# Optimization experiments

Hardware: AMD Instinct MI355X
Metric: run time of the kernel (lower is better)

Reference implementation:

```python
import jax, jax.numpy as jnp
import numpy as np

B, S, D = 2, 2048, 1024
H, DQK, DV = 16, 64, 64
DECAY = 0.85


def _fractal_weights(seq_len: int, decay: float) -> np.ndarray:
    # Dragon-curve hierarchical weights: earlier (coarser) positions get higher
    # weight; weight decays by `decay` per hierarchy level. Normalized to sum 1,
    # matching DragonCurveGenerator.get_hierarchical_weights semantics.
    idx = np.arange(seq_len)
    level = np.floor(np.log2(idx + 1)).astype(np.int32)
    w = decay ** level.astype(np.float32)
    return (w / w.sum()).astype(np.float32)


def setup_inputs() -> dict:
    key = jax.random.key(0)
    kx, kq, kk, kv, ko = jax.random.split(key, 5)
    s = 1.0 / np.sqrt(D)
    return {
        "x": jax.random.normal(kx, (B, S, D), dtype=jnp.float32),
        "Wq": jax.random.normal(kq, (D, H * DQK), dtype=jnp.float32) * s,
        "Wk": jax.random.normal(kk, (D, H * DQK), dtype=jnp.float32) * s,
        "Wv": jax.random.normal(kv, (D, H * DV), dtype=jnp.float32) * s,
        "Wo": jax.random.normal(ko, (H * DV, D), dtype=jnp.float32) * s,
        "fractal_weights": jnp.asarray(_fractal_weights(S, DECAY)),
    }


def reference(x, Wq, Wk, Wv, Wo, fractal_weights):
    b, s, _ = x.shape
    # Projections (Linear with bias=False); weights stored as (in, out).
    Q = (x @ Wq).reshape(b, s, H, DQK).transpose(0, 2, 1, 3)  # [B,H,S,Dqk]
    K = (x @ Wk).reshape(b, s, H, DQK).transpose(0, 2, 1, 3)
    V = (x @ Wv).reshape(b, s, H, DV).transpose(0, 2, 1, 3)   # [B,H,S,Dv]
    scale = 1.0 / jnp.sqrt(jnp.asarray(DQK, dtype=x.dtype))
    scores = jnp.einsum("bhqd,bhkd->bhqk", Q, K) * scale      # [B,H,S,S]
    # Multiplicative per-key fractal bias applied BEFORE softmax.
    scores = scores * fractal_weights[None, None, None, :]
    attn = jax.nn.softmax(scores, axis=-1)
    out = jnp.einsum("bhqk,bhkd->bhqd", attn, V)               # [B,H,S,Dv]
    out = out.transpose(0, 2, 1, 3).reshape(b, s, H * DV)
    return out @ Wo                                            # [B,S,D]
```

## Files before the change

### kernel.cpp

```cpp
#include <hip/hip_runtime.h>
#include <hip/hip_bf16.h>
#include <stdint.h>

#define B_  2
#define S_  2048
#define D_  1024
#define H_  16
#define DH_ 64

typedef __attribute__((ext_vector_type(8))) __bf16    bf16x8;
typedef __attribute__((ext_vector_type(8))) _Float16  f16x8;
typedef __attribute__((ext_vector_type(4))) _Float16  f16x4;
typedef __attribute__((ext_vector_type(2))) __fp16    fp16x2;
typedef __attribute__((ext_vector_type(4))) float     f32x4;

__device__ inline unsigned short f2bf(float f) {
    union { float f; uint32_t u; } v; v.f = f;
    uint32_t r = (v.u + 0x7fffu + ((v.u >> 16) & 1u)) >> 16;
    return (unsigned short)r;
}

__device__ __forceinline__ void g2l16(const unsigned short* g, unsigned short* l) {
    __builtin_amdgcn_global_load_lds(
        (const __attribute__((address_space(1))) unsigned int*)g,
        (__attribute__((address_space(3))) unsigned int*)l,
        16, 0, 0);
}


__global__ void convert_x(const float* __restrict__ x, unsigned short* __restrict__ xb, int n) {
    int i = (blockIdx.x * blockDim.x + threadIdx.x) * 4;
    if (i < n) {
        float4 v = *(const float4*)(x + i);
        ushort4 o;
        o.x = f2bf(v.x); o.y = f2bf(v.y); o.z = f2bf(v.z); o.w = f2bf(v.w);
        *(ushort4*)(xb + i) = o;
    }
}

__global__ void transpose_w(const float* __restrict__ s0, const float* __restrict__ s1,
                            const float* __restrict__ s2, const float* __restrict__ s3,
                            unsigned short* __restrict__ d0, unsigned short* __restrict__ d1,
                            unsigned short* __restrict__ d2, unsigned short* __restrict__ d3) {
    __shared__ float tile[32][33];
    const float* src; unsigned short* dst;
    switch (blockIdx.z) {
        case 0: src = s0; dst = d0; break;
        case 1: src = s1; dst = d1; break;
        case 2: src = s2; dst = d2; break;
        default: src = s3; dst = d3; break;
    }
    int n0 = blockIdx.x * 32, k0 = blockIdx.y * 32;
    int tx = threadIdx.x, ty = threadIdx.y;
    for (int j = 0; j < 32; j += 8)
        tile[ty + j][tx] = src[(long)(k0 + ty + j) * 1024 + n0 + tx];
    __syncthreads();
    for (int j = 0; j < 32; j += 8)
        dst[(long)(n0 + ty + j) * 1024 + k0 + tx] = f2bf(tile[tx][ty + j]);
}

__global__ __launch_bounds__(256, 2)
void gemm128(const unsigned short* __restrict__ A, const unsigned short* __restrict__ Bt,
             unsigned short* __restrict__ Qo, unsigned short* __restrict__ Ko,
             unsigned short* __restrict__ Vt,
             const float* __restrict__ fw)
{
    __shared__ __align__(16) unsigned short As[128 * 64];
    __shared__ __align__(16) unsigned short Bs[128 * 64];
    const int tid  = threadIdx.x;
    const int lane = tid & 63, wid = tid >> 6;
    const int quad = lane >> 4, l15 = lane & 15;
    const int wm = wid >> 1, wn = wid & 1;
    const int bm = blockIdx.y, bn = blockIdx.x;
    const int K = 1024;
    f32x4 acc[4][4] = {};
    const long Abase = (long)bm * 128 * K;
    const long Bbase = (long)bn * 128 * K;

    for (int k0 = 0; k0 < K; k0 += 64) {
        __syncthreads();
#pragma unroll
        for (int i = 0; i < 4; i++) {
            int slot = i * 256 + wid * 64 + lane;
            int row = slot >> 3, cp = slot & 7;
            int c = cp ^ (row & 7);
            g2l16(A + Abase + (long)row * K + k0 + c * 8, &As[(i * 256 + wid * 64) * 8]);
        }
#pragma unroll
        for (int i = 0; i < 4; i++) {
            int slot = i * 256 + wid * 64 + lane;
            int row = slot >> 3, cp = slot & 7;
            int c = cp ^ (row & 7);
            g2l16(Bt + Bbase + (long)row * K + k0 + c * 8, &Bs[(i * 256 + wid * 64) * 8]);
        }
        __syncthreads();
#pragma unroll
        for (int ks = 0; ks < 2; ks++) {
            bf16x8 af[4], bfr[4];
#pragma unroll
            for (int t = 0; t < 4; t++) {
                int ra = wm * 64 + t * 16 + l15;
                af[t]  = *(const bf16x8*)(As + ra * 64 + (((ks * 4 + quad) ^ (l15 & 7))) * 8);
                int rb = wn * 64 + t * 16 + l15;
                bfr[t] = *(const bf16x8*)(Bs + rb * 64 + (((ks * 4 + quad) ^ (l15 & 7))) * 8);
            }
#pragma unroll
            for (int tm = 0; tm < 4; tm++)
#pragma unroll
                for (int tn = 0; tn < 4; tn++)
                    acc[tm][tn] = __builtin_amdgcn_mfma_f32_16x16x32_bf16(af[tm], bfr[tn], acc[tm][tn], 0, 0, 0);
        }
    }

    const float Cq = 0.125f * 1.44269504f;
    for (int tm = 0; tm < 4; tm++)
        for (int tn = 0; tn < 4; tn++)
            for (int r = 0; r < 4; r++) {
                int gm = bm * 128 + wm * 64 + tm * 16 + quad * 4 + r;
                int gn = bn * 128 + wn * 64 + tn * 16 + l15;
                float v = acc[tm][tn][r];
                int b = gm >> 11, s = gm & 2047;
                if (gn < 1024) {
                    int h = gn >> 6, d = gn & 63;
                    Qo[(((long)(b * H_ + h) * S_ + s) << 6) + d] = f2bf(v * Cq);
                } else if (gn < 2048) {
                    int g = gn - 1024; int h = g >> 6, d = g & 63;
                    Ko[(((long)(b * H_ + h) * S_ + s) << 6) + d] = f2bf(v * fw[s]);
                } else {
                    int g = gn - 2048; int h = g >> 6, d = g & 63;
                    union { _Float16 h; unsigned short u; } cv;
                    cv.h = (_Float16)v;
                    int sp = s ^ ((d & 8) ? 4 : 0);
                    Vt[((long)(b * H_ + h) * DH_ + d) * S_ + sp] = cv.u;
                }
            }
}

__global__ __launch_bounds__(256, 2)
void gemm_wo(const unsigned short* __restrict__ A, const unsigned short* __restrict__ Bt,
             float* __restrict__ Cout)
{
    __shared__ __align__(16) unsigned short As[128 * 64];
    __shared__ __align__(16) unsigned short Bs[64 * 64];
    const int tid  = threadIdx.x;
    const int lane = tid & 63, wid = tid >> 6;
    const int quad = lane >> 4, l15 = lane & 15;
    const int bm = blockIdx.y, bn = blockIdx.x;
    const int K = 1024;
    f32x4 acc[2][4] = {};
    const long Abase = (long)bm * 128 * K;
    const long Bbase = (long)bn * 64 * K;

    for (int k0 = 0; k0 < K; k0 += 64) {
        __syncthreads();
#pragma unroll
        for (int i = 0; i < 4; i++) {
            int slot = i * 256 + wid * 64 + lane;
            int row = slot >> 3, cp = slot & 7;
            int c = cp ^ (row & 7);
            g2l16(A + Abase + (long)row * K + k0 + c * 8, &As[(i * 256 + wid * 64) * 8]);
        }
#pragma unroll
        for (int i = 0; i < 2; i++) {
            int slot = i * 256 + wid * 64 + lane;
            int row = slot >> 3, cp = slot & 7;
            int c = cp ^ (row & 7);
            g2l16(Bt + Bbase + (long)row * K + k0 + c * 8, &Bs[(i * 256 + wid * 64) * 8]);
        }
        __syncthreads();
#pragma unroll
        for (int ks = 0; ks < 2; ks++) {
            bf16x8 af[2], bfr[4];
#pragma unroll
            for (int t = 0; t < 2; t++) {
                int ra = wid * 32 + t * 16 + l15;
                af[t]  = *(const bf16x8*)(As + ra * 64 + (((ks * 4 + quad) ^ (l15 & 7))) * 8);
            }
#pragma unroll
            for (int t = 0; t < 4; t++) {
                int rb = t * 16 + l15;
                bfr[t] = *(const bf16x8*)(Bs + rb * 64 + (((ks * 4 + quad) ^ (l15 & 7))) * 8);
            }
#pragma unroll
            for (int tm = 0; tm < 2; tm++)
#pragma unroll
                for (int tn = 0; tn < 4; tn++)
                    acc[tm][tn] = __builtin_amdgcn_mfma_f32_16x16x32_bf16(af[tm], bfr[tn], acc[tm][tn], 0, 0, 0);
        }
    }

    for (int tm = 0; tm < 2; tm++)
        for (int tn = 0; tn < 4; tn++)
            for (int r = 0; r < 4; r++) {
                int gm = bm * 128 + wid * 32 + tm * 16 + quad * 4 + r;
                int gn = bn * 64 + tn * 16 + l15;
                Cout[(long)gm * 1024 + gn] = acc[tm][tn][r];
            }
}

__global__ __launch_bounds__(512, 4)
void attn_kernel(const unsigned short* __restrict__ Q, const unsigned short* __restrict__ Kb,
                 const unsigned short* __restrict__ Vt,
                 unsigned short* __restrict__ O)
{
    __shared__ __align__(16) unsigned short smem[2][2][2][64 * 64];

    const int tid  = threadIdx.x;
    const int lane = tid & 63, wid = tid >> 6;
    const int half = wid >> 2, sw = wid & 3;
    const int quad = lane >> 4, l15 = lane & 15;
    const int bh = blockIdx.y;
    const int qt = blockIdx.x;

    const unsigned short* Kg = Kb + (long)bh * S_ * DH_;
    const unsigned short* Vg = Vt + (long)bh * (long)DH_ * S_;

    bf16x8 qf[2][2];
#pragma unroll
    for (int st = 0; st < 2; st++) {
        const unsigned short* Qp = Q + ((long)bh * S_ + qt * 128 + sw * 32 + st * 16 + l15) * DH_ + quad * 8;
        qf[st][0] = *(const bf16x8*)(Qp);
        qf[st][1] = *(const bf16x8*)(Qp + 32);
    }

    auto issue = [&](int buf, int kt) {
#pragma unroll
        for (int i = 0; i < 2; i++) {
            int base = i * 256 + sw * 64;
            int slot = base + lane;
            int row = slot >> 3, cp = slot & 7;
            int c = cp ^ (row & 7);
            g2l16(Kg + ((long)(kt * 64 + row) * 64 + c * 8), &smem[half][buf][0][base * 8]);
        }
#pragma unroll
        for (int i = 0; i < 2; i++) {
            int base = i * 256 + sw * 64;
            int slot = base + lane;
            int row = slot >> 3, cp = slot & 7;
            int c = cp ^ (row & 7);
            g2l16(Vg + ((long)row * S_ + kt * 64 + c * 8), &smem[half][buf][1][base * 8]);
        }
    };

    f32x4 oacc[2][4] = {};
    f32x4 lacc[2] = {};
    const f16x8 vone = {(_Float16)1.f, (_Float16)1.f, (_Float16)1.f, (_Float16)1.f,
                        (_Float16)1.f, (_Float16)1.f, (_Float16)1.f, (_Float16)1.f};

    const int kt0 = half * 16;
    issue(0, kt0);
    __syncthreads();

    const int hf = (((quad & 1) ^ ((l15 >> 3) & 1))) * 4;

    for (int t = 0; t < 16; t++) {
        const int cur = t & 1;
        if (t + 1 < 16) issue(1 - cur, kt0 + t + 1);

        const unsigned short* Kc = &smem[half][cur][0][0];
        const unsigned short* Vc = &smem[half][cur][1][0];

        f32x4 sacc[2][4] = {};
#pragma unroll
        for (int kc = 0; kc < 4; kc++) {
            int row = kc * 16 + l15;
            bf16x8 k0 = *(const bf16x8*)(Kc + (row * 8 + (quad       ^ (l15 & 7))) * 8);
            bf16x8 k1 = *(const bf16x8*)(Kc + (row * 8 + ((4 + quad) ^ (l15 & 7))) * 8);
#pragma unroll
            for (int st = 0; st < 2; st++) {
                sacc[st][kc] = __builtin_amdgcn_mfma_f32_16x16x32_bf16(k0, qf[st][0], sacc[st][kc], 0, 0, 0);
                sacc[st][kc] = __builtin_amdgcn_mfma_f32_16x16x32_bf16(k1, qf[st][1], sacc[st][kc], 0, 0, 0);
            }
        }

        f16x8 vfr[2][4];
#pragma unroll
        for (int c = 0; c < 2; c++)
#pragma unroll
            for (int dt = 0; dt < 4; dt++) {
                int row = dt * 16 + l15;
                int p0 = (c * 4 +     (quad >> 1)) ^ (l15 & 7);
                int p1 = (c * 4 + 2 + (quad >> 1)) ^ (l15 & 7);
                f16x4 v0 = *(const f16x4*)(Vc + row * 64 + p0 * 8 + hf);
                f16x4 v1 = *(const f16x4*)(Vc + row * 64 + p1 * 8 + hf);
                vfr[c][dt] = __builtin_shufflevector(v0, v1, 0, 1, 2, 3, 4, 5, 6, 7);
            }

        f16x8 pk8[2][2];
#pragma unroll
        for (int st = 0; st < 2; st++)
#pragma unroll
            for (int c = 0; c < 2; c++) {
                union { uint4 u; f16x8 v; } pku;
#pragma unroll
                for (int hh = 0; hh < 2; hh++) {
                    float p0 = __builtin_amdgcn_exp2f(sacc[st][2 * c + hh][0]);
                    float p1 = __builtin_amdgcn_exp2f(sacc[st][2 * c + hh][1]);
                    float p2 = __builtin_amdgcn_exp2f(sacc[st][2 * c + hh][2]);
                    float p3 = __builtin_amdgcn_exp2f(sacc[st][2 * c + hh][3]);
                    union { fp16x2 h2; unsigned int u; } a, b;
                    a.h2 = __builtin_amdgcn_cvt_pkrtz(p0, p1);
                    b.h2 = __builtin_amdgcn_cvt_pkrtz(p2, p3);
                    if (hh == 0) { pku.u.x = a.u; pku.u.y = b.u; }
                    else         { pku.u.z = a.u; pku.u.w = b.u; }
                }
                pk8[st][c] = pku.v;
            }

#pragma unroll
        for (int c = 0; c < 2; c++) {
            lacc[0] = __builtin_amdgcn_mfma_f32_16x16x32_f16(pk8[0][c], vone, lacc[0], 0, 0, 0);
            lacc[1] = __builtin_amdgcn_mfma_f32_16x16x32_f16(pk8[1][c], vone, lacc[1], 0, 0, 0);
#pragma unroll
            for (int dt = 0; dt < 4; dt++) {
                oacc[0][dt] = __builtin_amdgcn_mfma_f32_16x16x32_f16(pk8[0][c], vfr[c][dt], oacc[0][dt], 0, 0, 0);
                oacc[1][dt] = __builtin_amdgcn_mfma_f32_16x16x32_f16(pk8[1][c], vfr[c][dt], oacc[1][dt], 0, 0, 0);
            }
        }

        __syncthreads();
    }

    float* ov = (float*)&smem[0][0][0][0];
    float* lv = ov + 128 * 66;

    if (half == 1) {
#pragma unroll
        for (int st = 0; st < 2; st++) {
#pragma unroll
            for (int dt = 0; dt < 4; dt++)
#pragma unroll
                for (int r = 0; r < 4; r++) {
                    int qr = sw * 32 + st * 16 + quad * 4 + r;
                    ov[qr * 66 + dt * 16 + l15] = oacc[st][dt][r];
                }
            if (l15 == 0) {
#pragma unroll
                for (int r = 0; r < 4; r++)
                    lv[sw * 32 + st * 16 + quad * 4 + r] = lacc[st][r];
            }
        }
    }
    __syncthreads();

    if (half == 0) {
        int b = bh >> 4, h = bh & 15;
#pragma unroll
        for (int st = 0; st < 2; st++)
#pragma unroll
            for (int r = 0; r < 4; r++) {
                int qr = sw * 32 + st * 16 + quad * 4 + r;
                float inv = 1.0f / (lacc[st][r] + lv[qr]);
                int srow = qt * 128 + qr;
#pragma unroll
                for (int dt = 0; dt < 4; dt++) {
                    float val = oacc[st][dt][r] + ov[qr * 66 + dt * 16 + l15];
                    O[((long)(b * S_ + srow)) * 1024 + h * DH_ + dt * 16 + l15] = f2bf(val * inv);
                }
            }
    }
}


extern "C" void kernel_launch(void* const* d_in, const int* in_sizes, int n_in,
                              void* d_out, int out_size, void* d_ws, size_t ws_size,
                              hipStream_t stream)
{
    const float* x  = (const float*)d_in[0];
    const float* Wq = (const float*)d_in[1];
    const float* Wk = (const float*)d_in[2];
    const float* Wv = (const float*)d_in[3];
    const float* Wo = (const float*)d_in[4];
    const float* fw = (const float*)d_in[5];
    float* out = (float*)d_out;

    char* ws = (char*)d_ws;
    unsigned short* xb    = (unsigned short*)(ws);
    unsigned short* WqkvT = (unsigned short*)(ws + 8388608);
    unsigned short* WoT   = (unsigned short*)(ws + 14680064);
    unsigned short* Qb    = (unsigned short*)(ws + 16777216);
    unsigned short* Kb    = (unsigned short*)(ws + 25165824);
    unsigned short* Vt    = (unsigned short*)(ws + 33554432);
    unsigned short* Ob    = xb;

    convert_x<<<dim3((B_ * S_ * D_) / 4 / 256), dim3(256), 0, stream>>>(x, xb, B_ * S_ * D_);
    transpose_w<<<dim3(32, 32, 4), dim3(32, 8), 0, stream>>>(
        Wq, Wk, Wv, Wo,
        WqkvT, WqkvT + 1024 * 1024, WqkvT + 2 * 1024 * 1024, WoT);
    gemm128<<<dim3(24, 32), dim3(256), 0, stream>>>(xb, WqkvT, Qb, Kb, Vt, fw);
    attn_kernel<<<dim3(S_ / 128, B_ * H_), dim3(512), 0, stream>>>(Qb, Kb, Vt, Ob);
    gemm_wo<<<dim3(16, 32), dim3(256), 0, stream>>>(Ob, WoT, out);
}
```

Baseline: 188.7 us.

## Double-buffer LDS tiles in QKV and output projection GEMMs

Both projection GEMMs now keep two shared-memory buffers for the A and B tiles. The next K-slice is prefetched with global_load_lds into the idle buffer while MFMAs run on the current one, and one barrier per iteration replaces two. The aim is to hide global-to-LDS load latency behind matrix math. In exchange, LDS use per block doubles, which may limit occupancy, and correctness relies on the barrier waiting for the async loads to land.

```diff
diff --git a/kernel.cpp b/kernel.cpp
--- a/kernel.cpp
+++ b/kernel.cpp
@@ -65,8 +65,8 @@
              unsigned short* __restrict__ Vt,
              const float* __restrict__ fw)
 {
-    __shared__ __align__(16) unsigned short As[128 * 64];
-    __shared__ __align__(16) unsigned short Bs[128 * 64];
+    __shared__ __align__(16) unsigned short As[2][128 * 64];
+    __shared__ __align__(16) unsigned short Bs[2][128 * 64];
     const int tid  = threadIdx.x;
     const int lane = tid & 63, wid = tid >> 6;
     const int quad = lane >> 4, l15 = lane & 15;
@@ -77,32 +77,38 @@
     const long Abase = (long)bm * 128 * K;
     const long Bbase = (long)bn * 128 * K;
 
-    for (int k0 = 0; k0 < K; k0 += 64) {
-        __syncthreads();
+    auto stage = [&](int buf, int k0) {
 #pragma unroll
         for (int i = 0; i < 4; i++) {
             int slot = i * 256 + wid * 64 + lane;
             int row = slot >> 3, cp = slot & 7;
             int c = cp ^ (row & 7);
-            g2l16(A + Abase + (long)row * K + k0 + c * 8, &As[(i * 256 + wid * 64) * 8]);
+            g2l16(A + Abase + (long)row * K + k0 + c * 8, &As[buf][(i * 256 + wid * 64) * 8]);
         }
 #pragma unroll
         for (int i = 0; i < 4; i++) {
             int slot = i * 256 + wid * 64 + lane;
             int row = slot >> 3, cp = slot & 7;
             int c = cp ^ (row & 7);
-            g2l16(Bt + Bbase + (long)row * K + k0 + c * 8, &Bs[(i * 256 + wid * 64) * 8]);
-        }
-        __syncthreads();
+            g2l16(Bt + Bbase + (long)row * K + k0 + c * 8, &Bs[buf][(i * 256 + wid * 64) * 8]);
+        }
+    };
+
+    stage(0, 0);
+    __syncthreads();
+
+    for (int t = 0; t < 16; t++) {
+        const int cur = t & 1;
+        if (t + 1 < 16) stage(1 - cur, (t + 1) * 64);
 #pragma unroll
         for (int ks = 0; ks < 2; ks++) {
             bf16x8 af[4], bfr[4];
 #pragma unroll
-            for (int t = 0; t < 4; t++) {
-                int ra = wm * 64 + t * 16 + l15;
-                af[t]  = *(const bf16x8*)(As + ra * 64 + (((ks * 4 + quad) ^ (l15 & 7))) * 8);
-                int rb = wn * 64 + t * 16 + l15;
-                bfr[t] = *(const bf16x8*)(Bs + rb * 64 + (((ks * 4 + quad) ^ (l15 & 7))) * 8);
+            for (int tt = 0; tt < 4; tt++) {
+                int ra = wm * 64 + tt * 16 + l15;
+                af[tt]  = *(const bf16x8*)(&As[cur][0] + ra * 64 + (((ks * 4 + quad) ^ (l15 & 7))) * 8);
+                int rb = wn * 64 + tt * 16 + l15;
+                bfr[tt] = *(const bf16x8*)(&Bs[cur][0] + rb * 64 + (((ks * 4 + quad) ^ (l15 & 7))) * 8);
             }
 #pragma unroll
             for (int tm = 0; tm < 4; tm++)
@@ -110,6 +116,7 @@
                 for (int tn = 0; tn < 4; tn++)
                     acc[tm][tn] = __builtin_amdgcn_mfma_f32_16x16x32_bf16(af[tm], bfr[tn], acc[tm][tn], 0, 0, 0);
         }
+        __syncthreads();
     }
 
     const float Cq = 0.125f * 1.44269504f;
@@ -140,8 +147,8 @@
 void gemm_wo(const unsigned short* __restrict__ A, const unsigned short* __restrict__ Bt,
              float* __restrict__ Cout)
 {
-    __shared__ __align__(16) unsigned short As[128 * 64];
-    __shared__ __align__(16) unsigned short Bs[64 * 64];
+    __shared__ __align__(16) unsigned short As[2][128 * 64];
+    __shared__ __align__(16) unsigned short Bs[2][64 * 64];
     const int tid  = threadIdx.x;
     const int lane = tid & 63, wid = tid >> 6;
     const int quad = lane >> 4, l15 = lane & 15;
@@ -151,35 +158,41 @@
     const long Abase = (long)bm * 128 * K;
     const long Bbase = (long)bn * 64 * K;
 
-    for (int k0 = 0; k0 < K; k0 += 64) {
-        __syncthreads();
+    auto stage = [&](int buf, int k0) {
 #pragma unroll
         for (int i = 0; i < 4; i++) {
             int slot = i * 256 + wid * 64 + lane;
             int row = slot >> 3, cp = slot & 7;
             int c = cp ^ (row & 7);
-            g2l16(A + Abase + (long)row * K + k0 + c * 8, &As[(i * 256 + wid * 64) * 8]);
+            g2l16(A + Abase + (long)row * K + k0 + c * 8, &As[buf][(i * 256 + wid * 64) * 8]);
         }
 #pragma unroll
         for (int i = 0; i < 2; i++) {
             int slot = i * 256 + wid * 64 + lane;
             int row = slot >> 3, cp = slot & 7;
             int c = cp ^ (row & 7);
-            g2l16(Bt + Bbase + (long)row * K + k0 + c * 8, &Bs[(i * 256 + wid * 64) * 8]);
-        }
-        __syncthreads();
+            g2l16(Bt + Bbase + (long)row * K + k0 + c * 8, &Bs[buf][(i * 256 + wid * 64) * 8]);
+        }
+    };
+
+    stage(0, 0);
+    __syncthreads();
+
+    for (int t = 0; t < 16; t++) {
+        const int cur = t & 1;
+        if (t + 1 < 16) stage(1 - cur, (t + 1) * 64);
 #pragma unroll
         for (int ks = 0; ks < 2; ks++) {
             bf16x8 af[2], bfr[4];
 #pragma unroll
-            for (int t = 0; t < 2; t++) {
-                int ra = wid * 32 + t * 16 + l15;
-                af[t]  = *(const bf16x8*)(As + ra * 64 + (((ks * 4 + quad) ^ (l15 & 7))) * 8);
-            }
-#pragma unroll
-            for (int t = 0; t < 4; t++) {
-                int rb = t * 16 + l15;
-                bfr[t] = *(const bf16x8*)(Bs + rb * 64 + (((ks * 4 + quad) ^ (l15 & 7))) * 8);
+            for (int tt = 0; tt < 2; tt++) {
+                int ra = wid * 32 + tt * 16 + l15;
+                af[tt]  = *(const bf16x8*)(&As[cur][0] + ra * 64 + (((ks * 4 + quad) ^ (l15 & 7))) * 8);
+            }
+#pragma unroll
+            for (int tt = 0; tt < 4; tt++) {
+                int rb = tt * 16 + l15;
+                bfr[tt] = *(const bf16x8*)(&Bs[cur][0] + rb * 64 + (((ks * 4 + quad) ^ (l15 & 7))) * 8);
             }
 #pragma unroll
             for (int tm = 0; tm < 2; tm++)
@@ -187,6 +200,7 @@
                 for (int tn = 0; tn < 4; tn++)
                     acc[tm][tn] = __builtin_amdgcn_mfma_f32_16x16x32_bf16(af[tm], bfr[tn], acc[tm][tn], 0, 0, 0);
         }
+        __syncthreads();
     }
 
     for (int tm = 0; tm < 2; tm++)
```

New measurement: 203.4 us. 1.08x slower.
